# Kernel optimization log

Hardware: AMD Instinct MI355X
Metric: run time of the kernel (lower is better)

Reference implementation:

```python
import jax, jax.numpy as jnp
import numpy as np

N = 50000   # nodes
E = 800000  # edges (before self loops)
XD, PD, H = 3, 3, 64
EPS = 1e-5


def setup_inputs() -> dict:
    key = jax.random.key(0)
    ks = jax.random.split(key, 24)
    def rn(k, shape, scale=1.0):
        return jax.random.normal(k, shape, dtype=jnp.float32) * scale
    inp = {
        'x': rn(ks[0], (N, XD)),
        'pos': rn(ks[1], (N, PD)),
        # MLP(6 -> 64 -> 64 -> 128), Linear+BN(+ReLU, last ReLU stripped)
        'W1': rn(ks[2], (XD + PD, H), 0.3), 'b1': rn(ks[3], (H,), 0.1),
        'g1': jax.random.uniform(ks[4], (H,), jnp.float32, 0.5, 1.5),
        'be1': rn(ks[5], (H,), 0.1), 'm1': rn(ks[6], (H,), 0.1),
        'v1': jax.random.uniform(ks[7], (H,), jnp.float32, 0.5, 1.5),
        'W2': rn(ks[8], (H, H), 0.1), 'b2': rn(ks[9], (H,), 0.1),
        'g2': jax.random.uniform(ks[10], (H,), jnp.float32, 0.5, 1.5),
        'be2': rn(ks[11], (H,), 0.1), 'm2': rn(ks[12], (H,), 0.1),
        'v2': jax.random.uniform(ks[13], (H,), jnp.float32, 0.5, 1.5),
        'W3': rn(ks[14], (H, 2 * H), 0.1), 'b3': rn(ks[15], (2 * H,), 0.1),
        'g3': jax.random.uniform(ks[16], (2 * H,), jnp.float32, 0.5, 1.5),
        'be3': rn(ks[17], (2 * H,), 0.1), 'm3': rn(ks[18], (2 * H,), 0.1),
        'v3': jax.random.uniform(ks[19], (2 * H,), jnp.float32, 0.5, 1.5),
        'edge_index': jax.random.randint(ks[20], (2, E), 0, N, dtype=jnp.int64),
    }
    return inp


def _bn(h, g, b, m, v):
    # inference-mode BatchNorm1d
    return (h - m) * jax.lax.rsqrt(v + EPS) * g + b


def reference(x, pos, W1, b1, g1, be1, m1, v1, W2, b2, g2, be2, m2, v2,
              W3, b3, g3, be3, m3, v3, edge_index):
    n = x.shape[0]
    loops = jnp.arange(n, dtype=edge_index.dtype)
    src = jnp.concatenate([edge_index[0], loops])  # j (source/neighbor)
    dst = jnp.concatenate([edge_index[1], loops])  # i (target)
    # per-edge feature: [x_j, pos_j - pos_i]  -> [E+N, 6]
    feat = jnp.concatenate([x[src], pos[src] - pos[dst]], axis=-1)
    h = jax.nn.relu(_bn(feat @ W1 + b1, g1, be1, m1, v1))
    h = jax.nn.relu(_bn(h @ W2 + b2, g2, be2, m2, v2))
    h = _bn(h @ W3 + b3, g3, be3, m3, v3)  # final ReLU stripped by MLP(modules[:-1])
    # max aggregation to destination nodes (PointNetConv default aggr='max')
    out = jax.ops.segment_max(h, dst, num_segments=n)
    return out
```

## Files before the change

kernel.cpp:

```cpp
#include <hip/hip_runtime.h>

#define N_NODES 50000
#define N_EDGES 800000
#define TOT_E   (N_EDGES + N_NODES)
#define EPS     1e-5f
#define SCAN_NB 196

typedef unsigned short u16;
typedef short v8s __attribute__((ext_vector_type(8)));
typedef float v4f __attribute__((ext_vector_type(4)));

#define WS_W1H    0
#define WS_W1L    4096
#define WS_W2H    8192
#define WS_W2L    16384
#define WS_W3H    24576
#define WS_W3L    40960
#define WS_B1F    57344
#define WS_B2F    57600
#define WS_B3F    57856
#define WS_BSUM   58368
#define WS_CURSOR 59392
#define WS_EID    259392

__device__ __forceinline__ unsigned rne_bf16(float f) {
    unsigned u = __float_as_uint(f);
    return (u + 0x7fffu + ((u >> 16) & 1u)) >> 16;
}

#define MFMA3(acc, ah, al, bh, bl)                                           \
    acc = __builtin_amdgcn_mfma_f32_16x16x32_bf16(ah, bh, acc, 0, 0, 0);     \
    acc = __builtin_amdgcn_mfma_f32_16x16x32_bf16(ah, bl, acc, 0, 0, 0);     \
    acc = __builtin_amdgcn_mfma_f32_16x16x32_bf16(al, bh, acc, 0, 0, 0);

__global__ void fold_kernel(
    const float* __restrict__ W1, const float* __restrict__ b1,
    const float* __restrict__ g1, const float* __restrict__ be1,
    const float* __restrict__ m1, const float* __restrict__ v1,
    const float* __restrict__ W2, const float* __restrict__ b2,
    const float* __restrict__ g2, const float* __restrict__ be2,
    const float* __restrict__ m2, const float* __restrict__ v2,
    const float* __restrict__ W3, const float* __restrict__ b3,
    const float* __restrict__ g3, const float* __restrict__ be3,
    const float* __restrict__ m3, const float* __restrict__ v3,
    u16* __restrict__ w1h, u16* __restrict__ w1l,
    u16* __restrict__ w2h, u16* __restrict__ w2l,
    u16* __restrict__ w3h, u16* __restrict__ w3l,
    float* __restrict__ b1f, float* __restrict__ b2f, float* __restrict__ b3f)
{
    int t = blockIdx.x * blockDim.x + threadIdx.x;
    float val = 0.f;
    u16 *ph = nullptr, *pl = nullptr;
    int idx = 0;
    if (t < 2048) {
        int n = t >> 5, k = t & 31;
        float s = g1[n] * rsqrtf(v1[n] + EPS);
        val = (k < 6) ? W1[k * 64 + n] * s : 0.f;
        ph = w1h; pl = w1l; idx = t;
    } else if (t < 6144) {
        int i = t - 2048; int n = i >> 6, k = i & 63;
        float s = g2[n] * rsqrtf(v2[n] + EPS);
        val = W2[k * 64 + n] * s;
        ph = w2h; pl = w2l; idx = i;
    } else if (t < 14336) {
        int i = t - 6144; int n = i >> 6, k = i & 63;
        float s = g3[n] * rsqrtf(v3[n] + EPS);
        val = W3[k * 128 + n] * s;
        ph = w3h; pl = w3l; idx = i;
    } else if (t < 14592) {
        int i = t - 14336;
        if (i < 64) {
            float s = g1[i] * rsqrtf(v1[i] + EPS);
            b1f[i] = (b1[i] - m1[i]) * s + be1[i];
        } else if (i < 128) {
            int j = i - 64;
            float s = g2[j] * rsqrtf(v2[j] + EPS);
            b2f[j] = (b2[j] - m2[j]) * s + be2[j];
        } else {
            int j = i - 128;
            float s = g3[j] * rsqrtf(v3[j] + EPS);
            b3f[j] = (b3[j] - m3[j]) * s + be3[j];
        }
        return;
    } else return;
    unsigned hi = rne_bf16(val);
    unsigned lo = rne_bf16(val - __uint_as_float(hi << 16));
    ph[idx] = (u16)hi;
    pl[idx] = (u16)lo;
}

__global__ void init_kernel(int* __restrict__ cursor, uint4* __restrict__ out4) {
    int i = blockIdx.x * 256 + threadIdx.x;
    if (i < N_NODES) cursor[i] = 1;
    if (i < (N_NODES * 128) / 4)
        out4[i] = make_uint4(0xFF800000u, 0xFF800000u, 0xFF800000u, 0xFF800000u);
}

__global__ void hist_kernel(const int* __restrict__ ei, int* __restrict__ cursor) {
    int e = blockIdx.x * 256 + threadIdx.x;
    if (e < N_EDGES) atomicAdd(&cursor[ei[N_EDGES + e]], 1);
}

__global__ void scanA_kernel(int* __restrict__ cursor, int* __restrict__ bsum) {
    __shared__ int sh[256];
    const int tid = threadIdx.x;
    int i = blockIdx.x * 256 + tid;
    int c = (i < N_NODES) ? cursor[i] : 0;
    sh[tid] = c;
    __syncthreads();
    int v = c;
    for (int off = 1; off < 256; off <<= 1) {
        int t = (tid >= off) ? sh[tid - off] : 0;
        __syncthreads();
        v += t;
        sh[tid] = v;
        __syncthreads();
    }
    if (i < N_NODES) cursor[i] = v - c;
    if (tid == 255) bsum[blockIdx.x] = v;
}

__global__ void scanB_kernel(int* __restrict__ bsum) {
    __shared__ int sh[256];
    const int tid = threadIdx.x;
    int c = (tid < SCAN_NB) ? bsum[tid] : 0;
    sh[tid] = c;
    __syncthreads();
    int v = c;
    for (int off = 1; off < 256; off <<= 1) {
        int t = (tid >= off) ? sh[tid - off] : 0;
        __syncthreads();
        v += t;
        sh[tid] = v;
        __syncthreads();
    }
    if (tid < SCAN_NB) bsum[tid] = v - c;
}

__global__ void scanC_kernel(int* __restrict__ cursor, const int* __restrict__ bsum) {
    int i = blockIdx.x * 256 + threadIdx.x;
    if (i < N_NODES) cursor[i] += bsum[blockIdx.x];
}

__global__ void scatter_kernel(const int* __restrict__ ei, int* __restrict__ cursor,
                               int* __restrict__ eid) {
    int e = blockIdx.x * 256 + threadIdx.x;
    if (e >= TOT_E) return;
    int d = (e < N_EDGES) ? ei[N_EDGES + e] : (e - N_EDGES);
    int p = atomicAdd(&cursor[d], 1);
    eid[p] = e;
}

__global__ __launch_bounds__(64, 2) void gather_kernel(
    const float* __restrict__ x, const float* __restrict__ pos,
    const int* __restrict__ ei, const int* __restrict__ eid,
    const u16* __restrict__ w1h, const u16* __restrict__ w1l,
    const u16* __restrict__ w2h, const u16* __restrict__ w2l,
    const u16* __restrict__ w3h, const u16* __restrict__ w3l,
    const float* __restrict__ b1f, const float* __restrict__ b2f,
    const float* __restrict__ b3f, float* __restrict__ out)
{
    __shared__ char smem[16384];

    const int lane = threadIdx.x;
    const int l15 = lane & 15, g = lane >> 4;
    const int e = blockIdx.x * 64 + lane;
    const bool active = e < TOT_E;

    int src = 0, dst = 0;
    if (active) {
        int id = eid[e];
        if (id < N_EDGES) { src = ei[id]; dst = ei[N_EDGES + id]; }
        else              { src = dst = id - N_EDGES; }
    }
    const int nid = active ? dst : (-1 - lane);

    const int np1 = __shfl_down(nid, 1);
    const bool seg_last = (lane == 63) || (np1 != nid);
    const unsigned long long segmask = __ballot(seg_last);

    float f0 = x[src * 3 + 0];
    float f1 = x[src * 3 + 1];
    float f2 = x[src * 3 + 2];
    float f3 = pos[src * 3 + 0] - pos[dst * 3 + 0];
    float f4 = pos[src * 3 + 1] - pos[dst * 3 + 1];
    float f5 = pos[src * 3 + 2] - pos[dst * 3 + 2];

    unsigned h0 = rne_bf16(f0), h1 = rne_bf16(f1), h2 = rne_bf16(f2);
    unsigned h3 = rne_bf16(f3), h4 = rne_bf16(f4), h5 = rne_bf16(f5);
    unsigned l0 = rne_bf16(f0 - __uint_as_float(h0 << 16));
    unsigned l1 = rne_bf16(f1 - __uint_as_float(h1 << 16));
    unsigned l2 = rne_bf16(f2 - __uint_as_float(h2 << 16));
    unsigned l3 = rne_bf16(f3 - __uint_as_float(h3 << 16));
    unsigned l4 = rne_bf16(f4 - __uint_as_float(h4 << 16));
    unsigned l5 = rne_bf16(f5 - __uint_as_float(h5 << 16));
    unsigned uh0 = h0 | (h1 << 16), uh1 = h2 | (h3 << 16), uh2 = h4 | (h5 << 16);
    unsigned ul0 = l0 | (l1 << 16), ul1 = l2 | (l3 << 16), ul2 = l4 | (l5 << 16);

    v8s a1h[4], a1l[4];
#pragma unroll
    for (int tm = 0; tm < 4; ++tm) {
        int bidx = (16 * tm + l15) * 4;
        unsigned p0 = (unsigned)__builtin_amdgcn_ds_bpermute(bidx, (int)uh0);
        unsigned p1 = (unsigned)__builtin_amdgcn_ds_bpermute(bidx, (int)uh1);
        unsigned p2 = (unsigned)__builtin_amdgcn_ds_bpermute(bidx, (int)uh2);
        unsigned q0 = (unsigned)__builtin_amdgcn_ds_bpermute(bidx, (int)ul0);
        unsigned q1 = (unsigned)__builtin_amdgcn_ds_bpermute(bidx, (int)ul1);
        unsigned q2 = (unsigned)__builtin_amdgcn_ds_bpermute(bidx, (int)ul2);
        if (g != 0) { p0 = p1 = p2 = q0 = q1 = q2 = 0u; }
        uint4 th = make_uint4(p0, p1, p2, 0u);
        uint4 tl = make_uint4(q0, q1, q2, 0u);
        a1h[tm] = __builtin_bit_cast(v8s, th);
        a1l[tm] = __builtin_bit_cast(v8s, tl);
    }

    v4f acc[4][4];
#pragma unroll
    for (int tn = 0; tn < 4; ++tn) {
        float bv = b1f[16 * tn + l15];
#pragma unroll
        for (int tm = 0; tm < 4; ++tm) acc[tm][tn] = (v4f){bv, bv, bv, bv};
    }
#pragma unroll
    for (int tn = 0; tn < 4; ++tn) {
        v8s bh = *(const v8s*)&w1h[(16 * tn + l15) * 32 + g * 8];
        v8s bl = *(const v8s*)&w1l[(16 * tn + l15) * 32 + g * 8];
#pragma unroll
        for (int tm = 0; tm < 4; ++tm) { MFMA3(acc[tm][tn], a1h[tm], a1l[tm], bh, bl) }
    }
#pragma unroll
    for (int tm = 0; tm < 4; ++tm)
#pragma unroll
        for (int tn = 0; tn < 4; ++tn)
#pragma unroll
            for (int r = 0; r < 4; ++r) {
                int row = 16 * tm + 4 * g + r, col = 16 * tn + l15;
                float v = fmaxf(acc[tm][tn][r], 0.f);
                unsigned hi = rne_bf16(v);
                unsigned lo = rne_bf16(v - __uint_as_float(hi << 16));
                int off = row * 128 + ((col * 2) ^ ((row & 7) << 4));
                *(u16*)(smem + off) = (u16)hi;
                *(u16*)(smem + 8192 + off) = (u16)lo;
            }

    v8s ah[4][2], al[4][2];
#pragma unroll
    for (int tm = 0; tm < 4; ++tm)
#pragma unroll
        for (int tk = 0; tk < 2; ++tk) {
            int row = 16 * tm + l15;
            int off = row * 128 + ((tk * 64 + g * 16) ^ ((row & 7) << 4));
            ah[tm][tk] = *(const v8s*)(smem + off);
            al[tm][tk] = *(const v8s*)(smem + 8192 + off);
        }

#pragma unroll
    for (int tn = 0; tn < 4; ++tn) {
        float bv = b2f[16 * tn + l15];
#pragma unroll
        for (int tm = 0; tm < 4; ++tm) acc[tm][tn] = (v4f){bv, bv, bv, bv};
    }
#pragma unroll
    for (int tn = 0; tn < 4; ++tn)
#pragma unroll
        for (int tk = 0; tk < 2; ++tk) {
            v8s bh = *(const v8s*)&w2h[(16 * tn + l15) * 64 + tk * 32 + g * 8];
            v8s bl = *(const v8s*)&w2l[(16 * tn + l15) * 64 + tk * 32 + g * 8];
#pragma unroll
            for (int tm = 0; tm < 4; ++tm) { MFMA3(acc[tm][tn], ah[tm][tk], al[tm][tk], bh, bl) }
        }
#pragma unroll
    for (int tm = 0; tm < 4; ++tm)
#pragma unroll
        for (int tn = 0; tn < 4; ++tn)
#pragma unroll
            for (int r = 0; r < 4; ++r) {
                int row = 16 * tm + 4 * g + r, col = 16 * tn + l15;
                float v = fmaxf(acc[tm][tn][r], 0.f);
                unsigned hi = rne_bf16(v);
                unsigned lo = rne_bf16(v - __uint_as_float(hi << 16));
                int off = row * 128 + ((col * 2) ^ ((row & 7) << 4));
                *(u16*)(smem + off) = (u16)hi;
                *(u16*)(smem + 8192 + off) = (u16)lo;
            }

#pragma unroll
    for (int tm = 0; tm < 4; ++tm)
#pragma unroll
        for (int tk = 0; tk < 2; ++tk) {
            int row = 16 * tm + l15;
            int off = row * 128 + ((tk * 64 + g * 16) ^ ((row & 7) << 4));
            ah[tm][tk] = *(const v8s*)(smem + off);
            al[tm][tk] = *(const v8s*)(smem + 8192 + off);
        }

#pragma unroll
    for (int h = 0; h < 2; ++h) {
#pragma unroll
        for (int tn = 0; tn < 4; ++tn) {
            float bv = b3f[64 * h + 16 * tn + l15];
#pragma unroll
            for (int tm = 0; tm < 4; ++tm) acc[tm][tn] = (v4f){bv, bv, bv, bv};
        }
#pragma unroll
        for (int tn = 0; tn < 4; ++tn)
#pragma unroll
            for (int tk = 0; tk < 2; ++tk) {
                int nrow = 16 * (4 * h + tn) + l15;
                v8s bh = *(const v8s*)&w3h[nrow * 64 + tk * 32 + g * 8];
                v8s bl = *(const v8s*)&w3l[nrow * 64 + tk * 32 + g * 8];
#pragma unroll
                for (int tm = 0; tm < 4; ++tm) { MFMA3(acc[tm][tn], ah[tm][tk], al[tm][tk], bh, bl) }
            }
#pragma unroll
        for (int tm = 0; tm < 4; ++tm)
#pragma unroll
            for (int tn = 0; tn < 4; ++tn)
#pragma unroll
                for (int r = 0; r < 4; ++r) {
                    int row = 16 * tm + 4 * g + r, col = 16 * tn + l15;
                    int off = row * 256 + ((col * 4) ^ ((row & 7) << 4));
                    *(float*)(smem + off) = acc[tm][tn][r];
                }

        {
            float runmax = -__builtin_inff();
            bool first = true;
#pragma unroll
            for (int e2 = 0; e2 < 64; ++e2) {
                int off = e2 * 256 + ((lane * 4) ^ ((e2 & 7) << 4));
                float val = *(const float*)(smem + off);
                runmax = fmaxf(runmax, val);
                if ((segmask >> e2) & 1ull) {
                    int n = __builtin_amdgcn_readlane(nid, e2);
                    if (n >= 0) {
                        float* op = out + (size_t)n * 128 + h * 64 + lane;
                        if (first || e2 == 63) atomicMax(op, runmax);
                        else *op = runmax;
                    }
                    first = false;
                    runmax = -__builtin_inff();
                }
            }
        }
    }
}

extern "C" void kernel_launch(void* const* d_in, const int* in_sizes, int n_in,
                              void* d_out, int out_size, void* d_ws, size_t ws_size,
                              hipStream_t stream) {
    const float* x   = (const float*)d_in[0];
    const float* pos = (const float*)d_in[1];
    const float* W1  = (const float*)d_in[2];
    const float* b1  = (const float*)d_in[3];
    const float* g1  = (const float*)d_in[4];
    const float* be1 = (const float*)d_in[5];
    const float* m1  = (const float*)d_in[6];
    const float* v1  = (const float*)d_in[7];
    const float* W2  = (const float*)d_in[8];
    const float* b2  = (const float*)d_in[9];
    const float* g2  = (const float*)d_in[10];
    const float* be2 = (const float*)d_in[11];
    const float* m2  = (const float*)d_in[12];
    const float* v2  = (const float*)d_in[13];
    const float* W3  = (const float*)d_in[14];
    const float* b3  = (const float*)d_in[15];
    const float* g3  = (const float*)d_in[16];
    const float* be3 = (const float*)d_in[17];
    const float* m3  = (const float*)d_in[18];
    const float* v3  = (const float*)d_in[19];
    const int*   ei  = (const int*)d_in[20];

    char* ws = (char*)d_ws;
    u16* w1h = (u16*)(ws + WS_W1H);
    u16* w1l = (u16*)(ws + WS_W1L);
    u16* w2h = (u16*)(ws + WS_W2H);
    u16* w2l = (u16*)(ws + WS_W2L);
    u16* w3h = (u16*)(ws + WS_W3H);
    u16* w3l = (u16*)(ws + WS_W3L);
    float* b1f = (float*)(ws + WS_B1F);
    float* b2f = (float*)(ws + WS_B2F);
    float* b3f = (float*)(ws + WS_B3F);
    int* bsum   = (int*)(ws + WS_BSUM);
    int* cursor = (int*)(ws + WS_CURSOR);
    int* eid    = (int*)(ws + WS_EID);
    float* outf = (float*)d_out;

    fold_kernel<<<57, 256, 0, stream>>>(
        W1, b1, g1, be1, m1, v1, W2, b2, g2, be2, m2, v2,
        W3, b3, g3, be3, m3, v3, w1h, w1l, w2h, w2l, w3h, w3l, b1f, b2f, b3f);

    init_kernel<<<(N_NODES * 128 / 4 + 255) / 256, 256, 0, stream>>>(
        cursor, (uint4*)d_out);

    hist_kernel<<<(N_EDGES + 255) / 256, 256, 0, stream>>>(ei, cursor);
    scanA_kernel<<<SCAN_NB, 256, 0, stream>>>(cursor, bsum);
    scanB_kernel<<<1, 256, 0, stream>>>(bsum);
    scanC_kernel<<<SCAN_NB, 256, 0, stream>>>(cursor, bsum);
    scatter_kernel<<<(TOT_E + 255) / 256, 256, 0, stream>>>(ei, cursor, eid);

    gather_kernel<<<(TOT_E + 63) / 64, 64, 0, stream>>>(
        x, pos, ei, eid, w1h, w1l, w2h, w2l, w3h, w3l, b1f, b2f, b3f, outf);
}
```

Before: 274.1 us.

## Halve gather LDS staging, fuse prep kernels, fold scan offset into scatter

The gather kernel's shared-memory buffer shrinks from 16 KB to 8 KB. Activations are now staged one half of K at a time, hi and lo halves share a row, and the layer-3 output is staged 32 rows at a time. Launch bounds rise to 3 waves per SIMD. Separately, the weight-fold and init kernels merge into one launch, and scanC is removed by adding the block offset inside scatter. This cuts launch overhead and LDS pressure to raise occupancy, but adds more LDS round-trips and separate accumulator arrays that may raise register pressure or cause spills.

```diff
diff --git a/kernel.cpp b/kernel.cpp
--- a/kernel.cpp
+++ b/kernel.cpp
@@ -33,7 +33,7 @@
     acc = __builtin_amdgcn_mfma_f32_16x16x32_bf16(ah, bl, acc, 0, 0, 0);     \
     acc = __builtin_amdgcn_mfma_f32_16x16x32_bf16(al, bh, acc, 0, 0, 0);
 
-__global__ void fold_kernel(
+__global__ void prep0_kernel(
     const float* __restrict__ W1, const float* __restrict__ b1,
     const float* __restrict__ g1, const float* __restrict__ be1,
     const float* __restrict__ m1, const float* __restrict__ v1,
@@ -46,54 +46,55 @@
     u16* __restrict__ w1h, u16* __restrict__ w1l,
     u16* __restrict__ w2h, u16* __restrict__ w2l,
     u16* __restrict__ w3h, u16* __restrict__ w3l,
-    float* __restrict__ b1f, float* __restrict__ b2f, float* __restrict__ b3f)
+    float* __restrict__ b1f, float* __restrict__ b2f, float* __restrict__ b3f,
+    int* __restrict__ cursor, uint4* __restrict__ out4)
 {
     int t = blockIdx.x * blockDim.x + threadIdx.x;
-    float val = 0.f;
-    u16 *ph = nullptr, *pl = nullptr;
-    int idx = 0;
-    if (t < 2048) {
-        int n = t >> 5, k = t & 31;
-        float s = g1[n] * rsqrtf(v1[n] + EPS);
-        val = (k < 6) ? W1[k * 64 + n] * s : 0.f;
-        ph = w1h; pl = w1l; idx = t;
-    } else if (t < 6144) {
-        int i = t - 2048; int n = i >> 6, k = i & 63;
-        float s = g2[n] * rsqrtf(v2[n] + EPS);
-        val = W2[k * 64 + n] * s;
-        ph = w2h; pl = w2l; idx = i;
-    } else if (t < 14336) {
-        int i = t - 6144; int n = i >> 6, k = i & 63;
-        float s = g3[n] * rsqrtf(v3[n] + EPS);
-        val = W3[k * 128 + n] * s;
-        ph = w3h; pl = w3l; idx = i;
-    } else if (t < 14592) {
-        int i = t - 14336;
-        if (i < 64) {
-            float s = g1[i] * rsqrtf(v1[i] + EPS);
-            b1f[i] = (b1[i] - m1[i]) * s + be1[i];
-        } else if (i < 128) {
-            int j = i - 64;
-            float s = g2[j] * rsqrtf(v2[j] + EPS);
-            b2f[j] = (b2[j] - m2[j]) * s + be2[j];
+
+    if (t < N_NODES) cursor[t] = 1;
+    if (t < (N_NODES * 128) / 4)
+        out4[t] = make_uint4(0xFF800000u, 0xFF800000u, 0xFF800000u, 0xFF800000u);
+
+    if (t < 14592) {
+        float val = 0.f;
+        u16 *ph = nullptr, *pl = nullptr;
+        int idx = 0;
+        if (t < 2048) {
+            int n = t >> 5, k = t & 31;
+            float s = g1[n] * rsqrtf(v1[n] + EPS);
+            val = (k < 6) ? W1[k * 64 + n] * s : 0.f;
+            ph = w1h; pl = w1l; idx = t;
+        } else if (t < 6144) {
+            int i = t - 2048; int n = i >> 6, k = i & 63;
+            float s = g2[n] * rsqrtf(v2[n] + EPS);
+            val = W2[k * 64 + n] * s;
+            ph = w2h; pl = w2l; idx = i;
+        } else if (t < 14336) {
+            int i = t - 6144; int n = i >> 6, k = i & 63;
+            float s = g3[n] * rsqrtf(v3[n] + EPS);
+            val = W3[k * 128 + n] * s;
+            ph = w3h; pl = w3l; idx = i;
         } else {
-            int j = i - 128;
-            float s = g3[j] * rsqrtf(v3[j] + EPS);
-            b3f[j] = (b3[j] - m3[j]) * s + be3[j];
+            int i = t - 14336;
+            if (i < 64) {
+                float s = g1[i] * rsqrtf(v1[i] + EPS);
+                b1f[i] = (b1[i] - m1[i]) * s + be1[i];
+            } else if (i < 128) {
+                int j = i - 64;
+                float s = g2[j] * rsqrtf(v2[j] + EPS);
+                b2f[j] = (b2[j] - m2[j]) * s + be2[j];
+            } else {
+                int j = i - 128;
+                float s = g3[j] * rsqrtf(v3[j] + EPS);
+                b3f[j] = (b3[j] - m3[j]) * s + be3[j];
+            }
+            return;
         }
-        return;
-    } else return;
-    unsigned hi = rne_bf16(val);
-    unsigned lo = rne_bf16(val - __uint_as_float(hi << 16));
-    ph[idx] = (u16)hi;
-    pl[idx] = (u16)lo;
-}
-
-__global__ void init_kernel(int* __restrict__ cursor, uint4* __restrict__ out4) {
-    int i = blockIdx.x * 256 + threadIdx.x;
-    if (i < N_NODES) cursor[i] = 1;
-    if (i < (N_NODES * 128) / 4)
-        out4[i] = make_uint4(0xFF800000u, 0xFF800000u, 0xFF800000u, 0xFF800000u);
+        unsigned hi = rne_bf16(val);
+        unsigned lo = rne_bf16(val - __uint_as_float(hi << 16));
+        ph[idx] = (u16)hi;
+        pl[idx] = (u16)lo;
+    }
 }
 
 __global__ void hist_kernel(const int* __restrict__ ei, int* __restrict__ cursor) {
@@ -137,21 +138,16 @@
     if (tid < SCAN_NB) bsum[tid] = v - c;
 }
 
-__global__ void scanC_kernel(int* __restrict__ cursor, const int* __restrict__ bsum) {
-    int i = blockIdx.x * 256 + threadIdx.x;
-    if (i < N_NODES) cursor[i] += bsum[blockIdx.x];
-}
-
 __global__ void scatter_kernel(const int* __restrict__ ei, int* __restrict__ cursor,
-                               int* __restrict__ eid) {
+                               const int* __restrict__ bsum, int* __restrict__ eid) {
     int e = blockIdx.x * 256 + threadIdx.x;
     if (e >= TOT_E) return;
     int d = (e < N_EDGES) ? ei[N_EDGES + e] : (e - N_EDGES);
     int p = atomicAdd(&cursor[d], 1);
-    eid[p] = e;
-}
-
-__global__ __launch_bounds__(64, 2) void gather_kernel(
+    eid[p + bsum[d >> 8]] = e;
+}
+
+__global__ __launch_bounds__(64, 3) void gather_kernel(
     const float* __restrict__ x, const float* __restrict__ pos,
     const int* __restrict__ ei, const int* __restrict__ eid,
     const u16* __restrict__ w1h, const u16* __restrict__ w1l,
@@ -160,7 +156,7 @@
     const float* __restrict__ b1f, const float* __restrict__ b2f,
     const float* __restrict__ b3f, float* __restrict__ out)
 {
-    __shared__ char smem[16384];
+    __shared__ char smem[8192];
 
     const int lane = threadIdx.x;
     const int l15 = lane & 15, g = lane >> 4;
@@ -228,79 +224,81 @@
 #pragma unroll
         for (int tm = 0; tm < 4; ++tm) { MFMA3(acc[tm][tn], a1h[tm], a1l[tm], bh, bl) }
     }
-#pragma unroll
-    for (int tm = 0; tm < 4; ++tm)
-#pragma unroll
-        for (int tn = 0; tn < 4; ++tn)
-#pragma unroll
-            for (int r = 0; r < 4; ++r) {
-                int row = 16 * tm + 4 * g + r, col = 16 * tn + l15;
-                float v = fmaxf(acc[tm][tn][r], 0.f);
-                unsigned hi = rne_bf16(v);
-                unsigned lo = rne_bf16(v - __uint_as_float(hi << 16));
-                int off = row * 128 + ((col * 2) ^ ((row & 7) << 4));
-                *(u16*)(smem + off) = (u16)hi;
-                *(u16*)(smem + 8192 + off) = (u16)lo;
-            }
-
-    v8s ah[4][2], al[4][2];
-#pragma unroll
-    for (int tm = 0; tm < 4; ++tm)
-#pragma unroll
-        for (int tk = 0; tk < 2; ++tk) {
-            int row = 16 * tm + l15;
-            int off = row * 128 + ((tk * 64 + g * 16) ^ ((row & 7) << 4));
-            ah[tm][tk] = *(const v8s*)(smem + off);
-            al[tm][tk] = *(const v8s*)(smem + 8192 + off);
-        }
-
+
+#define STAGE_HALF(ACC, tk)                                                      \
+    {                                                                            \
+        _Pragma("unroll")                                                        \
+        for (int t2 = 0; t2 < 2; ++t2) {                                         \
+            int tn = 2 * (tk) + t2;                                              \
+            _Pragma("unroll")                                                    \
+            for (int tm = 0; tm < 4; ++tm)                                       \
+                _Pragma("unroll")                                                \
+                for (int r = 0; r < 4; ++r) {                                    \
+                    int row = 16 * tm + 4 * g + r;                               \
+                    int f2 = 16 * t2 + l15;                                      \
+                    float v = fmaxf(ACC[tm][tn][r], 0.f);                        \
+                    unsigned hi = rne_bf16(v);                                   \
+                    unsigned lo = rne_bf16(v - __uint_as_float(hi << 16));       \
+                    int swz = (row & 7) << 4;                                    \
+                    *(u16*)(smem + row * 128 + ((f2 * 2) ^ swz)) = (u16)hi;      \
+                    *(u16*)(smem + row * 128 + ((64 + f2 * 2) ^ swz)) = (u16)lo; \
+                }                                                                \
+        }                                                                        \
+    }
+
+#define READ_FRAGS(AH, AL)                                                       \
+    {                                                                            \
+        _Pragma("unroll")                                                        \
+        for (int tm = 0; tm < 4; ++tm) {                                         \
+            int row = 16 * tm + l15;                                             \
+            int swz = (row & 7) << 4;                                            \
+            AH[tm] = *(const v8s*)(smem + row * 128 + ((g * 16) ^ swz));         \
+            AL[tm] = *(const v8s*)(smem + row * 128 + ((64 + g * 16) ^ swz));    \
+        }                                                                        \
+    }
+
+    v4f acc2[4][4];
 #pragma unroll
     for (int tn = 0; tn < 4; ++tn) {
         float bv = b2f[16 * tn + l15];
 #pragma unroll
-        for (int tm = 0; tm < 4; ++tm) acc[tm][tn] = (v4f){bv, bv, bv, bv};
-    }
-#pragma unroll
-    for (int tn = 0; tn < 4; ++tn)
-#pragma unroll
-        for (int tk = 0; tk < 2; ++tk) {
+        for (int tm = 0; tm < 4; ++tm) acc2[tm][tn] = (v4f){bv, bv, bv, bv};
+    }
+#pragma unroll
+    for (int tk = 0; tk < 2; ++tk) {
+        STAGE_HALF(acc, tk)
+        v8s ah[4], al[4];
+        READ_FRAGS(ah, al)
+#pragma unroll
+        for (int tn = 0; tn < 4; ++tn) {
             v8s bh = *(const v8s*)&w2h[(16 * tn + l15) * 64 + tk * 32 + g * 8];
             v8s bl = *(const v8s*)&w2l[(16 * tn + l15) * 64 + tk * 32 + g * 8];
 #pragma unroll
-            for (int tm = 0; tm < 4; ++tm) { MFMA3(acc[tm][tn], ah[tm][tk], al[tm][tk], bh, bl) }
+            for (int tm = 0; tm < 4; ++tm) { MFMA3(acc2[tm][tn], ah[tm], al[tm], bh, bl) }
         }
-#pragma unroll
-    for (int tm = 0; tm < 4; ++tm)
-#pragma unroll
-        for (int tn = 0; tn < 4; ++tn)
-#pragma unroll
-            for (int r = 0; r < 4; ++r) {
-                int row = 16 * tm + 4 * g + r, col = 16 * tn + l15;
-                float v = fmaxf(acc[tm][tn][r], 0.f);
-                unsigned hi = rne_bf16(v);
-                unsigned lo = rne_bf16(v - __uint_as_float(hi << 16));
-                int off = row * 128 + ((col * 2) ^ ((row & 7) << 4));
-                *(u16*)(smem + off) = (u16)hi;
-                *(u16*)(smem + 8192 + off) = (u16)lo;
-            }
-
-#pragma unroll
-    for (int tm = 0; tm < 4; ++tm)
-#pragma unroll
-        for (int tk = 0; tk < 2; ++tk) {
+    }
+
+    v8s ah3[4][2], al3[4][2];
+#pragma unroll
+    for (int tk = 0; tk < 2; ++tk) {
+        STAGE_HALF(acc2, tk)
+#pragma unroll
+        for (int tm = 0; tm < 4; ++tm) {
             int row = 16 * tm + l15;
-            int off = row * 128 + ((tk * 64 + g * 16) ^ ((row & 7) << 4));
-            ah[tm][tk] = *(const v8s*)(smem + off);
-            al[tm][tk] = *(const v8s*)(smem + 8192 + off);
+            int swz = (row & 7) << 4;
+            ah3[tm][tk] = *(const v8s*)(smem + row * 128 + ((g * 16) ^ swz));
+            al3[tm][tk] = *(const v8s*)(smem + row * 128 + ((64 + g * 16) ^ swz));
         }
+    }
 
 #pragma unroll
     for (int h = 0; h < 2; ++h) {
+        v4f acc3[4][4];
 #pragma unroll
         for (int tn = 0; tn < 4; ++tn) {
             float bv = b3f[64 * h + 16 * tn + l15];
 #pragma unroll
-            for (int tm = 0; tm < 4; ++tm) acc[tm][tn] = (v4f){bv, bv, bv, bv};
+            for (int tm = 0; tm < 4; ++tm) acc3[tm][tn] = (v4f){bv, bv, bv, bv};
         }
 #pragma unroll
         for (int tn = 0; tn < 4; ++tn)
@@ -310,25 +308,30 @@
                 v8s bh = *(const v8s*)&w3h[nrow * 64 + tk * 32 + g * 8];
                 v8s bl = *(const v8s*)&w3l[nrow * 64 + tk * 32 + g * 8];
 #pragma unroll
-                for (int tm = 0; tm < 4; ++tm) { MFMA3(acc[tm][tn], ah[tm][tk], al[tm][tk], bh, bl) }
+                for (int tm = 0; tm < 4; ++tm) { MFMA3(acc3[tm][tn], ah3[tm][tk], al3[tm][tk], bh, bl) }
             }
-#pragma unroll
-        for (int tm = 0; tm < 4; ++tm)
-#pragma unroll
-            for (int tn = 0; tn < 4; ++tn)
-#pragma unroll
-                for (int r = 0; r < 4; ++r) {
-                    int row = 16 * tm + 4 * g + r, col = 16 * tn + l15;
-                    int off = row * 256 + ((col * 4) ^ ((row & 7) << 4));
-                    *(float*)(smem + off) = acc[tm][tn][r];
-                }
-
-        {
-            float runmax = -__builtin_inff();
-            bool first = true;
-#pragma unroll
-            for (int e2 = 0; e2 < 64; ++e2) {
-                int off = e2 * 256 + ((lane * 4) ^ ((e2 & 7) << 4));
+
+        float runmax = -__builtin_inff();
+        bool first = true;
+#pragma unroll
+        for (int c = 0; c < 2; ++c) {
+#pragma unroll
+            for (int t2 = 0; t2 < 2; ++t2) {
+                int tm = 2 * c + t2;
+#pragma unroll
+                for (int tn = 0; tn < 4; ++tn)
+#pragma unroll
+                    for (int r = 0; r < 4; ++r) {
+                        int rl = 16 * t2 + 4 * g + r;
+                        int col = 16 * tn + l15;
+                        int off = rl * 256 + ((col * 4) ^ ((rl & 7) << 4));
+                        *(float*)(smem + off) = acc3[tm][tn][r];
+                    }
+            }
+#pragma unroll
+            for (int i = 0; i < 32; ++i) {
+                int e2 = 32 * c + i;
+                int off = i * 256 + ((lane * 4) ^ ((i & 7) << 4));
                 float val = *(const float*)(smem + off);
                 runmax = fmaxf(runmax, val);
                 if ((segmask >> e2) & 1ull) {
@@ -344,6 +347,8 @@
             }
         }
     }
+#undef STAGE_HALF
+#undef READ_FRAGS
 }
 
 extern "C" void kernel_launch(void* const* d_in, const int* in_sizes, int n_in,
@@ -386,18 +391,15 @@
     int* eid    = (int*)(ws + WS_EID);
     float* outf = (float*)d_out;
 
-    fold_kernel<<<57, 256, 0, stream>>>(
+    prep0_kernel<<<(N_NODES * 128 / 4 + 255) / 256, 256, 0, stream>>>(
         W1, b1, g1, be1, m1, v1, W2, b2, g2, be2, m2, v2,
-        W3, b3, g3, be3, m3, v3, w1h, w1l, w2h, w2l, w3h, w3l, b1f, b2f, b3f);
-
-    init_kernel<<<(N_NODES * 128 / 4 + 255) / 256, 256, 0, stream>>>(
-        cursor, (uint4*)d_out);
+        W3, b3, g3, be3, m3, v3, w1h, w1l, w2h, w2l, w3h, w3l,
+        b1f, b2f, b3f, cursor, (uint4*)d_out);
 
     hist_kernel<<<(N_EDGES + 255) / 256, 256, 0, stream>>>(ei, cursor);
     scanA_kernel<<<SCAN_NB, 256, 0, stream>>>(cursor, bsum);
     scanB_kernel<<<1, 256, 0, stream>>>(bsum);
-    scanC_kernel<<<SCAN_NB, 256, 0, stream>>>(cursor, bsum);
-    scatter_kernel<<<(TOT_E + 255) / 256, 256, 0, stream>>>(ei, cursor, eid);
+    scatter_kernel<<<(TOT_E + 255) / 256, 256, 0, stream>>>(ei, cursor, bsum, eid);
 
     gather_kernel<<<(TOT_E + 63) / 64, 64, 0, stream>>>(
         x, pos, ei, eid, w1h, w1l, w2h, w2l, w3h, w3l, b1f, b2f, b3f, outf);
```

New measurement: 333.3 us. +21.6%, slower.
